# Kernel optimization log

Hardware: AMD Instinct MI355X
Metric: run time of the kernel (lower is better)

The kernel has to match this reference:

```python
import jax, jax.numpy as jnp
import numpy as np

TOP_K = 8
ROUTED_SCALING_FACTOR = 1.5


def setup_inputs() -> dict:
    key = jax.random.key(0)
    k1, k2, k3 = jax.random.split(key, 3)
    T, D, E = 16384, 4096, 256  # tokens, hidden_size, n_routed_experts
    hidden_states = jax.random.normal(k1, (T, D), dtype=jnp.float32)
    W = jax.random.normal(k2, (E, D), dtype=jnp.float32) * (1.0 / np.sqrt(D))
    e_score_correction_bias = jax.random.normal(k3, (E,), dtype=jnp.float32) * 0.1
    return {"hidden_states": hidden_states, "W": W,
            "e_score_correction_bias": e_score_correction_bias}


def reference(hidden_states, W, e_score_correction_bias):
    # classifier: dense router GEMM [T, D] x [D, E] -> [T, E]
    classify_score = jnp.einsum('td,ed->te', hidden_states, W)
    # routing: softmax -> bias-corrected top-k selection -> gather of
    # UNbiased softmax scores, scaled.
    scores = jax.nn.softmax(classify_score, axis=-1)            # [T, E]
    scores_for_choice = scores + e_score_correction_bias[None]  # [T, E]
    _, topk_indices = jax.lax.top_k(scores_for_choice, TOP_K)   # [T, k]
    topk_weights = jnp.take_along_axis(scores, topk_indices, axis=-1)
    topk_weights = topk_weights.astype(jnp.float32) * ROUTED_SCALING_FACTOR
    return classify_score, topk_weights, topk_indices.astype(jnp.int32)
```

## Files before the change

kernel.cpp:

```cpp
#include <hip/hip_runtime.h>
#include <hip/hip_bf16.h>
#include <cstdint>


typedef __attribute__((ext_vector_type(8))) short short8;
typedef __attribute__((ext_vector_type(16))) float f32x16;

#define T_TOK  16384
#define DIM    4096
#define NE     256
#define TOPK_N 8

__device__ __forceinline__ float bf2f_u(unsigned short h) {
  return __uint_as_float(((unsigned int)h) << 16);
}
__device__ __forceinline__ unsigned cvt_pk2(float f0, float f1) {
  __hip_bfloat162 h2 = __float22bfloat162_rn(float2{f0, f1});
  unsigned u;
  __builtin_memcpy(&u, &h2, 4);
  return u;
}
__device__ __forceinline__ void split8(const float* f, uint4& hv, uint4& lv) {
  unsigned h[4], l[4];
#pragma unroll
  for (int c = 0; c < 4; ++c) {
    float a = f[2 * c], b = f[2 * c + 1];
    h[c] = cvt_pk2(a, b);
    float ra = a - bf2f_u((unsigned short)(h[c] & 0xffffu));
    float rb = b - bf2f_u((unsigned short)(h[c] >> 16));
    l[c] = cvt_pk2(ra, rb);
  }
  hv = uint4{h[0], h[1], h[2], h[3]};
  lv = uint4{l[0], l[1], l[2], l[3]};
}

__global__ __launch_bounds__(256) void convert_w_kernel(
    const float* __restrict__ W,
    unsigned short* __restrict__ Whp,
    unsigned short* __restrict__ Wlp) {
  const int t = blockIdx.x * 256 + threadIdx.x;
  const int e = t >> 9, k8 = t & 511;
  const int nt = e >> 5, col = e & 31;
  const int s = k8 >> 1, h = k8 & 1;
  const float* src = W + (size_t)e * DIM + k8 * 8;
  float f[8];
  *(float4*)(f)     = *(const float4*)src;
  *(float4*)(f + 4) = *(const float4*)(src + 4);
  uint4 hv, lv;
  split8(f, hv, lv);
  const size_t dst = ((size_t)(nt * 256 + s) * 64 + h * 32 + col) * 8;
  *(uint4*)(Whp + dst) = hv;
  *(uint4*)(Wlp + dst) = lv;
}

__device__ __forceinline__ f32x16 mfma32(short8 a, short8 b, f32x16 c) {
  return __builtin_amdgcn_mfma_f32_32x32x16_bf16(a, b, c, 0, 0, 0);
}

template <bool ATOMIC>
__global__ __launch_bounds__(512, 4) void gemm_router(
    const float* __restrict__ A,
    const unsigned short* __restrict__ Whp,
    const unsigned short* __restrict__ Wlp,
    float* C0,
    float* C1) {
  __shared__ __align__(16) unsigned short Ash[2][2][2][8][64][8];

  const int tid  = threadIdx.x;
  const int w    = tid >> 6, l = tid & 63;
  const int band = blockIdx.x & 255;
  const int kh   = blockIdx.x >> 8;
  const size_t kbase = (size_t)kh * 2048;
  float* C = (ATOMIC || kh == 0) ? C0 : C1;

  const int srow = tid >> 3, kg = tid & 7;
  const int smt = srow >> 5, sr = srow & 31;
  const float* ap = A + (size_t)(band * 64 + srow) * DIM + kbase + kg * 16;

  const unsigned short* ph = Whp + ((size_t)w * 256 + kh * 128) * 512 + (size_t)l * 8;
  const unsigned short* pl = Wlp + ((size_t)w * 256 + kh * 128) * 512 + (size_t)l * 8;

  f32x16 acc0 = {}, acc1 = {};
  float ar[16];

#pragma unroll
  for (int i = 0; i < 4; ++i)
    *(float4*)(ar + i * 4) = *(const float4*)(ap + i * 4);
  {
    uint4 hv0, lv0, hv1, lv1;
    split8(ar,     hv0, lv0);
    split8(ar + 8, hv1, lv1);
    *(uint4*)&Ash[0][0][smt][kg][ 0 + sr][0] = hv0;
    *(uint4*)&Ash[0][0][smt][kg][32 + sr][0] = hv1;
    *(uint4*)&Ash[0][1][smt][kg][ 0 + sr][0] = lv0;
    *(uint4*)&Ash[0][1][smt][kg][32 + sr][0] = lv1;
  }
#pragma unroll
  for (int i = 0; i < 4; ++i)
    *(float4*)(ar + i * 4) = *(const float4*)(ap + 128 + i * 4);

  short8 b[2][2];
  b[0][0] = *(const short8*)(ph);
  b[0][1] = *(const short8*)(pl);
  b[1][0] = *(const short8*)(ph + 512);
  b[1][1] = *(const short8*)(pl + 512);

  for (int c = 0; c < 16; ++c) {
    const int buf = c & 1;
    asm volatile("s_waitcnt lgkmcnt(0)" ::: "memory");
    __builtin_amdgcn_s_barrier();
    asm volatile("" ::: "memory");

#pragma unroll
    for (int ks = 0; ks < 8; ++ks) {
      const int gs = c * 8 + ks;
      short8 Bh = b[gs & 1][0], Bl = b[gs & 1][1];
      const size_t gp = (size_t)((gs + 2 < 128) ? gs + 2 : gs) * 512;
      b[gs & 1][0] = *(const short8*)(ph + gp);
      b[gs & 1][1] = *(const short8*)(pl + gp);

      short8 a0h = *(const short8*)&Ash[buf][0][0][ks][l][0];
      short8 a0l = *(const short8*)&Ash[buf][1][0][ks][l][0];
      short8 a1h = *(const short8*)&Ash[buf][0][1][ks][l][0];
      short8 a1l = *(const short8*)&Ash[buf][1][1][ks][l][0];

      __builtin_amdgcn_s_setprio(1);
      acc0 = mfma32(a0h, Bh, acc0);  acc1 = mfma32(a1h, Bh, acc1);
      acc0 = mfma32(a0l, Bh, acc0);  acc1 = mfma32(a1l, Bh, acc1);
      acc0 = mfma32(a0h, Bl, acc0);  acc1 = mfma32(a1h, Bl, acc1);
      __builtin_amdgcn_s_setprio(0);
    }

    if (c < 15) {
      {
        uint4 hv0, lv0, hv1, lv1;
        split8(ar,     hv0, lv0);
        split8(ar + 8, hv1, lv1);
        *(uint4*)&Ash[buf ^ 1][0][smt][kg][ 0 + sr][0] = hv0;
        *(uint4*)&Ash[buf ^ 1][0][smt][kg][32 + sr][0] = hv1;
        *(uint4*)&Ash[buf ^ 1][1][smt][kg][ 0 + sr][0] = lv0;
        *(uint4*)&Ash[buf ^ 1][1][smt][kg][32 + sr][0] = lv1;
      }
      if (c + 2 < 16) {
#pragma unroll
        for (int i = 0; i < 4; ++i)
          *(float4*)(ar + i * 4) = *(const float4*)(ap + (size_t)(c + 2) * 128 + i * 4);
      }
    }
  }

  const int rb = band * 64 + 4 * (l >> 5);
  const int cb = w * 32 + (l & 31);
#pragma unroll
  for (int r = 0; r < 16; ++r) {
    const int row = rb + (r & 3) + 8 * (r >> 2);
    if (ATOMIC) {
      unsafeAtomicAdd(&C[(size_t)row * NE + cb],        acc0[r]);
      unsafeAtomicAdd(&C[(size_t)(row + 32) * NE + cb], acc1[r]);
    } else {
      C[(size_t)row * NE + cb]        = acc0[r];
      C[(size_t)(row + 32) * NE + cb] = acc1[r];
    }
  }
}

template <bool FUSE>
__global__ __launch_bounds__(256) void topk_kernel(
    const float* __restrict__ Cp0, const float* __restrict__ Cp1,
    const float* __restrict__ bias, float* __restrict__ classify,
    float* __restrict__ wOut, float* __restrict__ iOut) {
  const int wave = threadIdx.x >> 6;
  const int lane = threadIdx.x & 63;
  const int tok  = blockIdx.x * 4 + wave;

  float4 c4 = *(const float4*)(Cp0 + (size_t)tok * NE + lane * 4);
  if (FUSE) {
    float4 p4 = *(const float4*)(Cp1 + (size_t)tok * NE + lane * 4);
    c4.x += p4.x; c4.y += p4.y; c4.z += p4.z; c4.w += p4.w;
    *(float4*)(classify + (size_t)tok * NE + lane * 4) = c4;
  }
  float v[4] = {c4.x, c4.y, c4.z, c4.w};

  float mx = fmaxf(fmaxf(v[0], v[1]), fmaxf(v[2], v[3]));
#pragma unroll
  for (int off = 32; off >= 1; off >>= 1) mx = fmaxf(mx, __shfl_xor(mx, off));

  float e0 = __expf(v[0] - mx), e1 = __expf(v[1] - mx);
  float e2 = __expf(v[2] - mx), e3 = __expf(v[3] - mx);
  float sum = e0 + e1 + e2 + e3;
#pragma unroll
  for (int off = 32; off >= 1; off >>= 1) sum += __shfl_xor(sum, off);

  float sc0 = e0 / sum, sc1 = e1 / sum, sc2 = e2 / sum, sc3 = e3 / sum;
  float4 b4 = *(const float4*)(bias + lane * 4);
  float ch0 = sc0 + b4.x, ch1 = sc1 + b4.y, ch2 = sc2 + b4.z, ch3 = sc3 + b4.w;

#pragma unroll
  for (int t = 0; t < TOPK_N; ++t) {
    float bv = ch0; int bi = 0; float bs = sc0;
    if (ch1 > bv) { bv = ch1; bi = 1; bs = sc1; }
    if (ch2 > bv) { bv = ch2; bi = 2; bs = sc2; }
    if (ch3 > bv) { bv = ch3; bi = 3; bs = sc3; }
    int be = lane * 4 + bi;
#pragma unroll
    for (int off = 32; off >= 1; off >>= 1) {
      float ov = __shfl_xor(bv, off);
      int   oe = __shfl_xor(be, off);
      float os = __shfl_xor(bs, off);
      if (ov > bv || (ov == bv && oe < be)) { bv = ov; be = oe; bs = os; }
    }
    if (lane == 0) {
      wOut[tok * TOPK_N + t] = bs * 1.5f;
      iOut[tok * TOPK_N + t] = (float)be;
    }
    bool own = (be >> 2) == lane;
    int  lb  = be & 3;
    if (own && lb == 0) ch0 = -INFINITY;
    if (own && lb == 1) ch1 = -INFINITY;
    if (own && lb == 2) ch2 = -INFINITY;
    if (own && lb == 3) ch3 = -INFINITY;
  }
}

extern "C" void kernel_launch(void* const* d_in, const int* in_sizes, int n_in,
                              void* d_out, int out_size, void* d_ws, size_t ws_size,
                              hipStream_t stream) {
  const float* hs   = (const float*)d_in[0];
  const float* W    = (const float*)d_in[1];
  const float* bias = (const float*)d_in[2];

  float* out      = (float*)d_out;
  float* classify = out;
  float* wOut     = out + (size_t)T_TOK * NE;
  float* iOut     = wOut + (size_t)T_TOK * TOPK_N;

  unsigned short* Whp = (unsigned short*)d_ws;
  unsigned short* Wlp = Whp + (size_t)NE * DIM;

  const size_t wpack_bytes = (size_t)NE * DIM * 2 * sizeof(unsigned short);
  const size_t part_bytes  = (size_t)T_TOK * NE * sizeof(float);
  float* p1 = (float*)((char*)d_ws + wpack_bytes);

  convert_w_kernel<<<(NE * DIM / 8) / 256, 256, 0, stream>>>(W, Whp, Wlp);

  if (ws_size >= wpack_bytes + part_bytes) {
    gemm_router<false><<<512, 512, 0, stream>>>(hs, Whp, Wlp, classify, p1);
    topk_kernel<true><<<T_TOK / 4, 256, 0, stream>>>(classify, p1, bias,
                                                     classify, wOut, iOut);
  } else {
    hipMemsetAsync(classify, 0, part_bytes, stream);
    gemm_router<true><<<512, 512, 0, stream>>>(hs, Whp, Wlp, classify, classify);
    topk_kernel<false><<<T_TOK / 4, 256, 0, stream>>>(classify, nullptr, bias,
                                                      classify, wOut, iOut);
  }
}
```

Baseline: 426.1 us.

## Fuse router GEMM with softmax/top-k epilogue and drop split-K

Replaces the split-K GEMM (512 blocks, two K halves writing partial outputs) plus a separate top-k kernel with a single kernel of 256 blocks. Each block covers the full K range, using two accumulator pairs, then stages the 64x256 tile in shared memory and runs softmax and bias-corrected top-k in place. This removes the partial-sum round trip through global memory and one kernel launch. In exchange it halves the grid to 256 blocks, which may leave compute units underused, and raises register pressure from the doubled accumulators.

```diff
diff --git a/kernel.cpp b/kernel.cpp
--- a/kernel.cpp
+++ b/kernel.cpp
@@ -57,30 +57,27 @@
   return __builtin_amdgcn_mfma_f32_32x32x16_bf16(a, b, c, 0, 0, 0);
 }
 
-template <bool ATOMIC>
-__global__ __launch_bounds__(512, 4) void gemm_router(
+__global__ __launch_bounds__(512, 2) void router_fused(
     const float* __restrict__ A,
     const unsigned short* __restrict__ Whp,
     const unsigned short* __restrict__ Wlp,
-    float* C0,
-    float* C1) {
+    const float* __restrict__ bias,
+    float* __restrict__ classify,
+    float* __restrict__ wOut, float* __restrict__ iOut) {
   __shared__ __align__(16) unsigned short Ash[2][2][2][8][64][8];
 
   const int tid  = threadIdx.x;
   const int w    = tid >> 6, l = tid & 63;
-  const int band = blockIdx.x & 255;
-  const int kh   = blockIdx.x >> 8;
-  const size_t kbase = (size_t)kh * 2048;
-  float* C = (ATOMIC || kh == 0) ? C0 : C1;
+  const int band = blockIdx.x;
 
   const int srow = tid >> 3, kg = tid & 7;
   const int smt = srow >> 5, sr = srow & 31;
-  const float* ap = A + (size_t)(band * 64 + srow) * DIM + kbase + kg * 16;
-
-  const unsigned short* ph = Whp + ((size_t)w * 256 + kh * 128) * 512 + (size_t)l * 8;
-  const unsigned short* pl = Wlp + ((size_t)w * 256 + kh * 128) * 512 + (size_t)l * 8;
-
-  f32x16 acc0 = {}, acc1 = {};
+  const float* ap = A + (size_t)(band * 64 + srow) * DIM + kg * 16;
+
+  const unsigned short* ph = Whp + (size_t)w * 256 * 512 + (size_t)l * 8;
+  const unsigned short* pl = Wlp + (size_t)w * 256 * 512 + (size_t)l * 8;
+
+  f32x16 accA0 = {}, accA1 = {}, accB0 = {}, accB1 = {};
   float ar[16];
 
 #pragma unroll
@@ -105,120 +102,113 @@
   b[1][0] = *(const short8*)(ph + 512);
   b[1][1] = *(const short8*)(pl + 512);
 
-  for (int c = 0; c < 16; ++c) {
-    const int buf = c & 1;
-    asm volatile("s_waitcnt lgkmcnt(0)" ::: "memory");
-    __builtin_amdgcn_s_barrier();
-    asm volatile("" ::: "memory");
-
-#pragma unroll
-    for (int ks = 0; ks < 8; ++ks) {
-      const int gs = c * 8 + ks;
-      short8 Bh = b[gs & 1][0], Bl = b[gs & 1][1];
-      const size_t gp = (size_t)((gs + 2 < 128) ? gs + 2 : gs) * 512;
-      b[gs & 1][0] = *(const short8*)(ph + gp);
-      b[gs & 1][1] = *(const short8*)(pl + gp);
-
-      short8 a0h = *(const short8*)&Ash[buf][0][0][ks][l][0];
-      short8 a0l = *(const short8*)&Ash[buf][1][0][ks][l][0];
-      short8 a1h = *(const short8*)&Ash[buf][0][1][ks][l][0];
-      short8 a1l = *(const short8*)&Ash[buf][1][1][ks][l][0];
-
-      __builtin_amdgcn_s_setprio(1);
-      acc0 = mfma32(a0h, Bh, acc0);  acc1 = mfma32(a1h, Bh, acc1);
-      acc0 = mfma32(a0l, Bh, acc0);  acc1 = mfma32(a1l, Bh, acc1);
-      acc0 = mfma32(a0h, Bl, acc0);  acc1 = mfma32(a1h, Bl, acc1);
-      __builtin_amdgcn_s_setprio(0);
+  auto half_loop = [&](int cbeg, f32x16& acc0, f32x16& acc1) {
+    for (int c = cbeg; c < cbeg + 16; ++c) {
+      const int buf = c & 1;
+      asm volatile("s_waitcnt lgkmcnt(0)" ::: "memory");
+      __builtin_amdgcn_s_barrier();
+      asm volatile("" ::: "memory");
+
+#pragma unroll
+      for (int ks = 0; ks < 8; ++ks) {
+        const int gs = c * 8 + ks;
+        short8 Bh = b[gs & 1][0], Bl = b[gs & 1][1];
+        const size_t gp = (size_t)((gs + 2 < 256) ? gs + 2 : gs) * 512;
+        b[gs & 1][0] = *(const short8*)(ph + gp);
+        b[gs & 1][1] = *(const short8*)(pl + gp);
+
+        short8 a0h = *(const short8*)&Ash[buf][0][0][ks][l][0];
+        short8 a0l = *(const short8*)&Ash[buf][1][0][ks][l][0];
+        short8 a1h = *(const short8*)&Ash[buf][0][1][ks][l][0];
+        short8 a1l = *(const short8*)&Ash[buf][1][1][ks][l][0];
+
+        __builtin_amdgcn_s_setprio(1);
+        acc0 = mfma32(a0h, Bh, acc0);  acc1 = mfma32(a1h, Bh, acc1);
+        acc0 = mfma32(a0l, Bh, acc0);  acc1 = mfma32(a1l, Bh, acc1);
+        acc0 = mfma32(a0h, Bl, acc0);  acc1 = mfma32(a1h, Bl, acc1);
+        __builtin_amdgcn_s_setprio(0);
+      }
+
+      if (c < 31) {
+        {
+          uint4 hv0, lv0, hv1, lv1;
+          split8(ar,     hv0, lv0);
+          split8(ar + 8, hv1, lv1);
+          *(uint4*)&Ash[buf ^ 1][0][smt][kg][ 0 + sr][0] = hv0;
+          *(uint4*)&Ash[buf ^ 1][0][smt][kg][32 + sr][0] = hv1;
+          *(uint4*)&Ash[buf ^ 1][1][smt][kg][ 0 + sr][0] = lv0;
+          *(uint4*)&Ash[buf ^ 1][1][smt][kg][32 + sr][0] = lv1;
+        }
+        if (c + 2 < 32) {
+#pragma unroll
+          for (int i = 0; i < 4; ++i)
+            *(float4*)(ar + i * 4) = *(const float4*)(ap + (size_t)(c + 2) * 128 + i * 4);
+        }
+      }
     }
-
-    if (c < 15) {
-      {
-        uint4 hv0, lv0, hv1, lv1;
-        split8(ar,     hv0, lv0);
-        split8(ar + 8, hv1, lv1);
-        *(uint4*)&Ash[buf ^ 1][0][smt][kg][ 0 + sr][0] = hv0;
-        *(uint4*)&Ash[buf ^ 1][0][smt][kg][32 + sr][0] = hv1;
-        *(uint4*)&Ash[buf ^ 1][1][smt][kg][ 0 + sr][0] = lv0;
-        *(uint4*)&Ash[buf ^ 1][1][smt][kg][32 + sr][0] = lv1;
-      }
-      if (c + 2 < 16) {
-#pragma unroll
-        for (int i = 0; i < 4; ++i)
-          *(float4*)(ar + i * 4) = *(const float4*)(ap + (size_t)(c + 2) * 128 + i * 4);
-      }
+  };
+  half_loop(0,  accA0, accA1);
+  half_loop(16, accB0, accB1);
+
+  __syncthreads();
+  float* Cl = (float*)Ash;
+
+  const int rbl = 4 * (l >> 5);
+  const int cb  = w * 32 + (l & 31);
+#pragma unroll
+  for (int r = 0; r < 16; ++r) {
+    const int rl = rbl + (r & 3) + 8 * (r >> 2);
+    Cl[(size_t)rl * NE + cb]        = accA0[r] + accB0[r];
+    Cl[(size_t)(rl + 32) * NE + cb] = accA1[r] + accB1[r];
+  }
+  __syncthreads();
+
+  const float4 b4 = *(const float4*)(bias + l * 4);
+  for (int i = 0; i < 8; ++i) {
+    const int rl  = w * 8 + i;
+    const int tok = band * 64 + rl;
+    float4 c4 = *(const float4*)&Cl[(size_t)rl * NE + l * 4];
+    *(float4*)(classify + (size_t)tok * NE + l * 4) = c4;
+    float v0 = c4.x, v1 = c4.y, v2 = c4.z, v3 = c4.w;
+
+    float mx = fmaxf(fmaxf(v0, v1), fmaxf(v2, v3));
+#pragma unroll
+    for (int off = 32; off >= 1; off >>= 1) mx = fmaxf(mx, __shfl_xor(mx, off));
+
+    float e0 = __expf(v0 - mx), e1 = __expf(v1 - mx);
+    float e2 = __expf(v2 - mx), e3 = __expf(v3 - mx);
+    float sum = e0 + e1 + e2 + e3;
+#pragma unroll
+    for (int off = 32; off >= 1; off >>= 1) sum += __shfl_xor(sum, off);
+
+    float sc0 = e0 / sum, sc1 = e1 / sum, sc2 = e2 / sum, sc3 = e3 / sum;
+    float ch0 = sc0 + b4.x, ch1 = sc1 + b4.y, ch2 = sc2 + b4.z, ch3 = sc3 + b4.w;
+
+#pragma unroll
+    for (int t = 0; t < TOPK_N; ++t) {
+      float bv = ch0; int bi = 0; float bs = sc0;
+      if (ch1 > bv) { bv = ch1; bi = 1; bs = sc1; }
+      if (ch2 > bv) { bv = ch2; bi = 2; bs = sc2; }
+      if (ch3 > bv) { bv = ch3; bi = 3; bs = sc3; }
+      int be = l * 4 + bi;
+#pragma unroll
+      for (int off = 32; off >= 1; off >>= 1) {
+        float ov = __shfl_xor(bv, off);
+        int   oe = __shfl_xor(be, off);
+        float os = __shfl_xor(bs, off);
+        if (ov > bv || (ov == bv && oe < be)) { bv = ov; be = oe; bs = os; }
+      }
+      if (l == 0) {
+        wOut[(size_t)tok * TOPK_N + t] = bs * 1.5f;
+        iOut[(size_t)tok * TOPK_N + t] = (float)be;
+      }
+      bool own = (be >> 2) == l;
+      int  lb  = be & 3;
+      if (own && lb == 0) ch0 = -INFINITY;
+      if (own && lb == 1) ch1 = -INFINITY;
+      if (own && lb == 2) ch2 = -INFINITY;
+      if (own && lb == 3) ch3 = -INFINITY;
     }
-  }
-
-  const int rb = band * 64 + 4 * (l >> 5);
-  const int cb = w * 32 + (l & 31);
-#pragma unroll
-  for (int r = 0; r < 16; ++r) {
-    const int row = rb + (r & 3) + 8 * (r >> 2);
-    if (ATOMIC) {
-      unsafeAtomicAdd(&C[(size_t)row * NE + cb],        acc0[r]);
-      unsafeAtomicAdd(&C[(size_t)(row + 32) * NE + cb], acc1[r]);
-    } else {
-      C[(size_t)row * NE + cb]        = acc0[r];
-      C[(size_t)(row + 32) * NE + cb] = acc1[r];
-    }
-  }
-}
-
-template <bool FUSE>
-__global__ __launch_bounds__(256) void topk_kernel(
-    const float* __restrict__ Cp0, const float* __restrict__ Cp1,
-    const float* __restrict__ bias, float* __restrict__ classify,
-    float* __restrict__ wOut, float* __restrict__ iOut) {
-  const int wave = threadIdx.x >> 6;
-  const int lane = threadIdx.x & 63;
-  const int tok  = blockIdx.x * 4 + wave;
-
-  float4 c4 = *(const float4*)(Cp0 + (size_t)tok * NE + lane * 4);
-  if (FUSE) {
-    float4 p4 = *(const float4*)(Cp1 + (size_t)tok * NE + lane * 4);
-    c4.x += p4.x; c4.y += p4.y; c4.z += p4.z; c4.w += p4.w;
-    *(float4*)(classify + (size_t)tok * NE + lane * 4) = c4;
-  }
-  float v[4] = {c4.x, c4.y, c4.z, c4.w};
-
-  float mx = fmaxf(fmaxf(v[0], v[1]), fmaxf(v[2], v[3]));
-#pragma unroll
-  for (int off = 32; off >= 1; off >>= 1) mx = fmaxf(mx, __shfl_xor(mx, off));
-
-  float e0 = __expf(v[0] - mx), e1 = __expf(v[1] - mx);
-  float e2 = __expf(v[2] - mx), e3 = __expf(v[3] - mx);
-  float sum = e0 + e1 + e2 + e3;
-#pragma unroll
-  for (int off = 32; off >= 1; off >>= 1) sum += __shfl_xor(sum, off);
-
-  float sc0 = e0 / sum, sc1 = e1 / sum, sc2 = e2 / sum, sc3 = e3 / sum;
-  float4 b4 = *(const float4*)(bias + lane * 4);
-  float ch0 = sc0 + b4.x, ch1 = sc1 + b4.y, ch2 = sc2 + b4.z, ch3 = sc3 + b4.w;
-
-#pragma unroll
-  for (int t = 0; t < TOPK_N; ++t) {
-    float bv = ch0; int bi = 0; float bs = sc0;
-    if (ch1 > bv) { bv = ch1; bi = 1; bs = sc1; }
-    if (ch2 > bv) { bv = ch2; bi = 2; bs = sc2; }
-    if (ch3 > bv) { bv = ch3; bi = 3; bs = sc3; }
-    int be = lane * 4 + bi;
-#pragma unroll
-    for (int off = 32; off >= 1; off >>= 1) {
-      float ov = __shfl_xor(bv, off);
-      int   oe = __shfl_xor(be, off);
-      float os = __shfl_xor(bs, off);
-      if (ov > bv || (ov == bv && oe < be)) { bv = ov; be = oe; bs = os; }
-    }
-    if (lane == 0) {
-      wOut[tok * TOPK_N + t] = bs * 1.5f;
-      iOut[tok * TOPK_N + t] = (float)be;
-    }
-    bool own = (be >> 2) == lane;
-    int  lb  = be & 3;
-    if (own && lb == 0) ch0 = -INFINITY;
-    if (own && lb == 1) ch1 = -INFINITY;
-    if (own && lb == 2) ch2 = -INFINITY;
-    if (own && lb == 3) ch3 = -INFINITY;
   }
 }
 
@@ -237,20 +227,7 @@
   unsigned short* Whp = (unsigned short*)d_ws;
   unsigned short* Wlp = Whp + (size_t)NE * DIM;
 
-  const size_t wpack_bytes = (size_t)NE * DIM * 2 * sizeof(unsigned short);
-  const size_t part_bytes  = (size_t)T_TOK * NE * sizeof(float);
-  float* p1 = (float*)((char*)d_ws + wpack_bytes);
-
   convert_w_kernel<<<(NE * DIM / 8) / 256, 256, 0, stream>>>(W, Whp, Wlp);
-
-  if (ws_size >= wpack_bytes + part_bytes) {
-    gemm_router<false><<<512, 512, 0, stream>>>(hs, Whp, Wlp, classify, p1);
-    topk_kernel<true><<<T_TOK / 4, 256, 0, stream>>>(classify, p1, bias,
-                                                     classify, wOut, iOut);
-  } else {
-    hipMemsetAsync(classify, 0, part_bytes, stream);
-    gemm_router<true><<<512, 512, 0, stream>>>(hs, Whp, Wlp, classify, classify);
-    topk_kernel<false><<<T_TOK / 4, 256, 0, stream>>>(classify, nullptr, bias,
-                                                      classify, wOut, iOut);
-  }
-}
+  router_fused<<<256, 512, 0, stream>>>(hs, Whp, Wlp, bias,
+                                        classify, wOut, iOut);
+}
```

After: 443.9 us. +4.2%, slower.
